# Kernel optimization log

Measured on AMD Instinct MI355X. Metric: run time of the kernel, lower is better.

Reference implementation:

```python
import jax, jax.numpy as jnp
import numpy as np

N = 100000   # nodes
E = 1600000  # edges
D = 256      # emb_dim
H = 512      # 2*emb_dim hidden in GIN MLP
L = 5        # num_layer
NUM_NODE_TYPES = 300
EDGE_FEAT = 7


def setup_inputs() -> dict:
    key = jax.random.key(0)
    ks = jax.random.split(key, 16)
    s = 0.05
    return {
        "x": jax.random.randint(ks[0], (N, 1), 0, NUM_NODE_TYPES, dtype=jnp.int32),
        "edge_index": jax.random.randint(ks[1], (2, E), 0, N, dtype=jnp.int32),
        "edge_attr": jax.random.normal(ks[2], (E, EDGE_FEAT), dtype=jnp.float32),
        "batch": jnp.zeros((N,), dtype=jnp.int32),
        "node_emb": jax.random.normal(ks[3], (NUM_NODE_TYPES, D), dtype=jnp.float32) * s,
        "We": jax.random.normal(ks[4], (L, EDGE_FEAT, D), dtype=jnp.float32) * s,
        "be": jnp.zeros((L, D), dtype=jnp.float32),
        "W1": jax.random.normal(ks[5], (L, D, H), dtype=jnp.float32) * s,
        "b1": jnp.zeros((L, H), dtype=jnp.float32),
        "g1": jnp.ones((L, H), dtype=jnp.float32),
        "bt1": jnp.zeros((L, H), dtype=jnp.float32),
        "W2": jax.random.normal(ks[6], (L, H, D), dtype=jnp.float32) * s,
        "b2": jnp.zeros((L, D), dtype=jnp.float32),
        "eps": jnp.zeros((L,), dtype=jnp.float32),
        "g_bn": jnp.ones((L, D), dtype=jnp.float32),
        "b_bn": jnp.zeros((L, D), dtype=jnp.float32),
    }


def _batchnorm(z, g, b):
    # training-mode BN over the node dim, biased variance, eps=1e-5 (torch default)
    mu = jnp.mean(z, axis=0)
    var = jnp.mean((z - mu) ** 2, axis=0)
    return (z - mu) * jax.lax.rsqrt(var + 1e-5) * g + b


def reference(x, edge_index, edge_attr, batch, node_emb, We, be, W1, b1, g1, bt1,
              W2, b2, eps, g_bn, b_bn):
    src, dst = edge_index[0], edge_index[1]
    h = node_emb[x[:, 0]]                      # [N, D]
    n = h.shape[0]
    for l in range(L):
        edge_emb = edge_attr @ We[l] + be[l]   # [E, D]
        msg = jax.nn.relu(h[src] + edge_emb)   # gather + elementwise message
        agg = jax.ops.segment_sum(msg, dst, num_segments=n)  # scatter-add
        z = (1.0 + eps[l]) * h + agg
        z = jax.nn.relu(_batchnorm(z @ W1[l] + b1[l], g1[l], bt1[l])) @ W2[l] + b2[l]
        z = _batchnorm(z, g_bn[l], b_bn[l])
        h = jax.nn.relu(z) if l != L - 1 else z  # relu on all but last; dropout p=0
    return h  # JK='last'
```

## Files before the change

kernel.cpp:

```cpp
#include <hip/hip_runtime.h>
#include <hip/hip_bf16.h>

#define N_NODES 100000
#define N_EDGES 1600000
#define DIM 256
#define HID 512
#define NLAYERS 5
#define BKP 40
#define MTILES 782

typedef unsigned short u16;
typedef unsigned int u32;
typedef short s16x8 __attribute__((ext_vector_type(8)));
typedef float f32x4 __attribute__((ext_vector_type(4)));

__device__ __forceinline__ float b2f_(u16 u) {
  union { unsigned i; float f; } v;
  v.i = ((unsigned)u) << 16;
  return v.f;
}
__device__ __forceinline__ u16 f2b_(float f) {
  __hip_bfloat16 h = __float2bfloat16(f);
  return *reinterpret_cast<u16*>(&h);
}
__device__ __forceinline__ int pk2_(u16 lo, u16 hi) {
  return (int)(((u32)hi << 16) | (u32)lo);
}
__device__ __forceinline__ void split_pack_(f32x4 a, f32x4 b, int4& hi, int4& lo) {
  float v[8];
  u16 h[8], l[8];
#pragma unroll
  for (int q = 0; q < 4; ++q) { v[q] = a[q]; v[4 + q] = b[q]; }
#pragma unroll
  for (int q = 0; q < 8; ++q) {
    h[q] = f2b_(v[q]);
    l[q] = f2b_(v[q] - b2f_(h[q]));
  }
  hi = make_int4(pk2_(h[0], h[1]), pk2_(h[2], h[3]), pk2_(h[4], h[5]), pk2_(h[6], h[7]));
  lo = make_int4(pk2_(l[0], l[1]), pk2_(l[2], l[3]), pk2_(l[4], l[5]), pk2_(l[6], l[7]));
}
__device__ __forceinline__ int4 bn_pack_(int4 raw, const float* __restrict__ scl,
                                         const float* __restrict__ sft) {
  const u16* rp = (const u16*)&raw;
  u16 o[8];
#pragma unroll
  for (int q = 0; q < 8; ++q) {
    float v = fmaf(b2f_(rp[q]), scl[q], sft[q]);
    o[q] = f2b_(fmaxf(v, 0.f));
  }
  return make_int4(pk2_(o[0], o[1]), pk2_(o[2], o[3]), pk2_(o[4], o[5]), pk2_(o[6], o[7]));
}

__global__ void k_fill(float* out, int n, float val) {
  int i = blockIdx.x * 256 + threadIdx.x;
  if (i < n) out[i] = val;
}

__global__ void k_zero(float* p, int n) {
  int i = blockIdx.x * 256 + threadIdx.x;
  if (i < n) p[i] = 0.f;
}

__global__ void k_zeroi(int* p, int n) {
  int i = blockIdx.x * 256 + threadIdx.x;
  if (i < n) p[i] = 0;
}

__global__ void k_gather(const int* x0, const int* x3, const float* emb, float* h) {
  int idx = blockIdx.x * 256 + threadIdx.x;
  int n = idx >> 8, d = idx & 255;
  int t = x0[n] + x3[n];
  h[idx] = emb[(size_t)t * DIM + d];
}

__global__ void k_hist(const int* __restrict__ dst, int* __restrict__ deg) {
  int e = blockIdx.x * 256 + threadIdx.x;
  if (e < N_EDGES) atomicAdd(&deg[dst[e]], 1);
}

__global__ void k_scan1(const int* __restrict__ deg, int* __restrict__ offs,
                        int* __restrict__ bsum) {
  __shared__ int sm[256];
  int tid = threadIdx.x;
  int i = blockIdx.x * 256 + tid;
  int v = (i < N_NODES) ? deg[i] : 0;
  sm[tid] = v;
  __syncthreads();
  for (int d = 1; d < 256; d <<= 1) {
    int t = (tid >= d) ? sm[tid - d] : 0;
    __syncthreads();
    sm[tid] += t;
    __syncthreads();
  }
  if (i < N_NODES) offs[i] = sm[tid] - v;
  if (tid == 0) bsum[blockIdx.x] = sm[255];
}

__global__ void k_scan2(int* __restrict__ bsum, int nb) {
  __shared__ int sm[512];
  int tid = threadIdx.x;
  int v = (tid < nb) ? bsum[tid] : 0;
  sm[tid] = v;
  __syncthreads();
  for (int d = 1; d < 512; d <<= 1) {
    int t = (tid >= d) ? sm[tid - d] : 0;
    __syncthreads();
    sm[tid] += t;
    __syncthreads();
  }
  if (tid < nb) bsum[tid] = sm[tid] - v;
}

__global__ void k_scan3(int* __restrict__ offs, const int* __restrict__ bsum,
                        int* __restrict__ cur) {
  int i = blockIdx.x * 256 + threadIdx.x;
  if (i < N_NODES) {
    offs[i] += bsum[blockIdx.x];
    cur[i] = 0;
  }
  if (i == 0) offs[N_NODES] = N_EDGES;
}

__global__ void k_fillcsr(const int* __restrict__ dst, const int* __restrict__ srcarr,
                          const float* __restrict__ ea, const int* __restrict__ offs,
                          int* __restrict__ cur, int* __restrict__ elist,
                          float* __restrict__ eaperm) {
  int e = blockIdx.x * 256 + threadIdx.x;
  if (e < N_EDGES) {
    int d = dst[e];
    int p = offs[d] + atomicAdd(&cur[d], 1);
    elist[p] = srcarr[e];
    const float* s = ea + (size_t)e * 7;
    float* o = eaperm + (size_t)p * 7;
#pragma unroll
    for (int k = 0; k < 7; ++k) o[k] = s[k];
  }
}

template <int BNIN>
__global__ __launch_bounds__(256) void k_agg(
    const float* __restrict__ hin, const float* __restrict__ eap,
    const int* __restrict__ csr, const int* __restrict__ offs,
    const float* __restrict__ We, const float* __restrict__ be,
    const float* __restrict__ eps_l, const float* __restrict__ scl2,
    const float* __restrict__ sft2, float* __restrict__ z) {
  const int lane = threadIdx.x & 63;
  const int n = blockIdx.x * 4 + (threadIdx.x >> 6);
  const int c0 = lane * 4;
  float w[7][4];
#pragma unroll
  for (int k = 0; k < 7; ++k) {
    f32x4 t = *(const f32x4*)&We[k * DIM + c0];
    w[k][0] = t[0]; w[k][1] = t[1]; w[k][2] = t[2]; w[k][3] = t[3];
  }
  const f32x4 bev = *(const f32x4*)&be[c0];
  f32x4 sv, fv;
  if (BNIN) { sv = *(const f32x4*)&scl2[c0]; fv = *(const f32x4*)&sft2[c0]; }
  const f32x4 hn = *(const f32x4*)&hin[(size_t)n * DIM + c0];
  const float e1p = 1.0f + eps_l[0];
  float acc[4];
#pragma unroll
  for (int q = 0; q < 4; ++q) {
    float hv = hn[q];
    if (BNIN) hv = fmaxf(fmaf(hv, sv[q], fv[q]), 0.f);
    acc[q] = e1p * hv;
  }

  auto msg = [&](const f32x4& hs, const float* a) {
#pragma unroll
    for (int q = 0; q < 4; ++q) {
      float hv = hs[q];
      if (BNIN) hv = fmaxf(fmaf(hv, sv[q], fv[q]), 0.f);
      float t = bev[q];
#pragma unroll
      for (int k = 0; k < 7; ++k) t = fmaf(a[k], w[k][q], t);
      acc[q] += fmaxf(hv + t, 0.f);
    }
  };

  const int eb = offs[n], ee = offs[n + 1];
  for (int base = eb; base < ee; base += 64) {
    const int m = min(64, ee - base);
    const int cs = csr[base + min(lane, m - 1)];
    int e = 0;
    for (; e + 4 <= m; e += 4) {
      const int s0 = __shfl(cs, e);
      const int s1 = __shfl(cs, e + 1);
      const int s2 = __shfl(cs, e + 2);
      const int s3 = __shfl(cs, e + 3);
      const f32x4 h0 = *(const f32x4*)&hin[(size_t)s0 * DIM + c0];
      const f32x4 h1 = *(const f32x4*)&hin[(size_t)s1 * DIM + c0];
      const f32x4 h2 = *(const f32x4*)&hin[(size_t)s2 * DIM + c0];
      const f32x4 h3 = *(const f32x4*)&hin[(size_t)s3 * DIM + c0];
      const float* p0 = eap + (size_t)(base + e) * 7;
      float a0[7], a1[7], a2[7], a3[7];
#pragma unroll
      for (int k = 0; k < 7; ++k) {
        a0[k] = p0[k]; a1[k] = p0[7 + k]; a2[k] = p0[14 + k]; a3[k] = p0[21 + k];
      }
      msg(h0, a0);
      msg(h1, a1);
      msg(h2, a2);
      msg(h3, a3);
    }
    for (; e < m; ++e) {
      const int s0 = __shfl(cs, e);
      const f32x4 h0 = *(const f32x4*)&hin[(size_t)s0 * DIM + c0];
      const float* p0 = eap + (size_t)(base + e) * 7;
      float a0[7];
#pragma unroll
      for (int k = 0; k < 7; ++k) a0[k] = p0[k];
      msg(h0, a0);
    }
  }
  f32x4 o;
#pragma unroll
  for (int q = 0; q < 4; ++q) o[q] = acc[q];
  *(f32x4*)&z[(size_t)n * DIM + c0] = o;
}

template <int K, int NC>
__global__ void k_wconv(const float* __restrict__ W, u16* __restrict__ Wth,
                        u16* __restrict__ Wtl) {
  int idx = blockIdx.x * 256 + threadIdx.x;
  int n = idx / K, k = idx - n * K;
  float w = W[(size_t)k * NC + n];
  u16 hh = f2b_(w);
  Wth[idx] = hh;
  Wtl[idx] = f2b_(w - b2f_(hh));
}

__global__ void k_bnprep(const float* __restrict__ sum, const float* __restrict__ sq,
                         const float* __restrict__ g, const float* __restrict__ bt,
                         float* __restrict__ scl, float* __restrict__ sft, int n) {
  int j = blockIdx.x * 256 + threadIdx.x;
  if (j < n) {
    const float invN = 1.0f / 100000.0f;
    float mu = sum[j] * invN;
    float var = fmaf(-mu, mu, sq[j] * invN);
    float s = g[j] * rsqrtf(var + 1e-5f);
    scl[j] = s;
    sft[j] = fmaf(-mu, s, bt[j]);
  }
}

template <int K, int NC, int NA, int OBF, int BN1A>
__global__ __launch_bounds__(256) void k_mgemm(
    const void* __restrict__ Av, const u16* __restrict__ Bth,
    const u16* __restrict__ Btl, const float* __restrict__ bias,
    void* __restrict__ Ov, float* __restrict__ colsum, float* __restrict__ colsq,
    const float* __restrict__ ascl, const float* __restrict__ asft) {
  __shared__ u16 As[NA * 128 * BKP];
  __shared__ u16 Bs[2 * 128 * BKP];
  const int tid = threadIdx.x;
  const int m0 = blockIdx.x * 128;
  const int n0 = blockIdx.y * 128;
  const int lane = tid & 63;
  const int wv = tid >> 6;
  const int wr = (wv >> 1) * 64;
  const int wc = (wv & 1) * 64;
  const int lr = lane & 15;
  const int kc = (lane >> 4) * 8;
  const int sr = tid >> 1;
  const int sc = (tid & 1) * 16;
  const int ga = min(m0 + sr, N_NODES - 1);
  const int gb = n0 + sr;

  const f32x4 z4 = {0.f, 0.f, 0.f, 0.f};
  f32x4 acc[4][4];
#pragma unroll
  for (int i = 0; i < 4; ++i)
#pragma unroll
    for (int j = 0; j < 4; ++j) acc[i][j] = z4;

  for (int k0 = 0; k0 < K; k0 += 32) {
    int4 a0, a1, al0, al1;
    if (NA == 2) {
      const float* src = (const float*)Av + (size_t)ga * K + k0 + sc;
      f32x4 v0 = *(const f32x4*)(src);
      f32x4 v1 = *(const f32x4*)(src + 4);
      f32x4 v2 = *(const f32x4*)(src + 8);
      f32x4 v3 = *(const f32x4*)(src + 12);
      split_pack_(v0, v1, a0, al0);
      split_pack_(v2, v3, a1, al1);
    } else {
      const u16* src = (const u16*)Av + (size_t)ga * K + k0 + sc;
      a0 = *(const int4*)(src);
      a1 = *(const int4*)(src + 8);
      if (BN1A) {
        a0 = bn_pack_(a0, ascl + k0 + sc, asft + k0 + sc);
        a1 = bn_pack_(a1, ascl + k0 + sc + 8, asft + k0 + sc + 8);
      }
    }
    const u16* bhp = Bth + (size_t)gb * K + k0 + sc;
    const u16* blp = Btl + (size_t)gb * K + k0 + sc;
    int4 b0 = *(const int4*)(bhp);
    int4 b1 = *(const int4*)(bhp + 8);
    int4 b2 = *(const int4*)(blp);
    int4 b3 = *(const int4*)(blp + 8);

    __syncthreads();
    *(int4*)&As[sr * BKP + sc] = a0;
    *(int4*)&As[sr * BKP + sc + 8] = a1;
    if (NA == 2) {
      *(int4*)&As[128 * BKP + sr * BKP + sc] = al0;
      *(int4*)&As[128 * BKP + sr * BKP + sc + 8] = al1;
    }
    *(int4*)&Bs[sr * BKP + sc] = b0;
    *(int4*)&Bs[sr * BKP + sc + 8] = b1;
    *(int4*)&Bs[128 * BKP + sr * BKP + sc] = b2;
    *(int4*)&Bs[128 * BKP + sr * BKP + sc + 8] = b3;
    __syncthreads();

    s16x8 aF[NA][4], bF[2][4];
#pragma unroll
    for (int i = 0; i < 4; ++i) {
      aF[0][i] = *reinterpret_cast<const s16x8*>(&As[(wr + i * 16 + lr) * BKP + kc]);
      if (NA == 2)
        aF[1][i] =
            *reinterpret_cast<const s16x8*>(&As[128 * BKP + (wr + i * 16 + lr) * BKP + kc]);
      bF[0][i] = *reinterpret_cast<const s16x8*>(&Bs[(wc + i * 16 + lr) * BKP + kc]);
      bF[1][i] = *reinterpret_cast<const s16x8*>(&Bs[128 * BKP + (wc + i * 16 + lr) * BKP + kc]);
    }
#pragma unroll
    for (int i = 0; i < 4; ++i)
#pragma unroll
      for (int j = 0; j < 4; ++j) {
        acc[i][j] =
            __builtin_amdgcn_mfma_f32_16x16x32_bf16(aF[0][i], bF[0][j], acc[i][j], 0, 0, 0);
        acc[i][j] =
            __builtin_amdgcn_mfma_f32_16x16x32_bf16(aF[0][i], bF[1][j], acc[i][j], 0, 0, 0);
        if (NA == 2)
          acc[i][j] =
              __builtin_amdgcn_mfma_f32_16x16x32_bf16(aF[1][i], bF[0][j], acc[i][j], 0, 0, 0);
      }
  }

  float bj[4];
#pragma unroll
  for (int j = 0; j < 4; ++j) bj[j] = bias[n0 + wc + j * 16 + lr];
  float ls[4] = {0.f, 0.f, 0.f, 0.f}, lq[4] = {0.f, 0.f, 0.f, 0.f};
#pragma unroll
  for (int i = 0; i < 4; ++i) {
    const int row0 = m0 + wr + i * 16 + (lane >> 4) * 4;
#pragma unroll
    for (int r = 0; r < 4; ++r) {
      const int grow = row0 + r;
      if (grow < N_NODES) {
        const size_t o = (size_t)grow * NC + n0 + wc + lr;
#pragma unroll
        for (int j = 0; j < 4; ++j) {
          float v = acc[i][j][r] + bj[j];
          ls[j] += v;
          lq[j] = fmaf(v, v, lq[j]);
          if (OBF) ((u16*)Ov)[o + j * 16] = f2b_(v);
          else ((float*)Ov)[o + j * 16] = v;
        }
      }
    }
  }
#pragma unroll
  for (int j = 0; j < 4; ++j) {
    float s = ls[j], q = lq[j];
    s += __shfl_xor(s, 16); q += __shfl_xor(q, 16);
    s += __shfl_xor(s, 32); q += __shfl_xor(q, 32);
    if ((lane >> 4) == 0) {
      unsafeAtomicAdd(&colsum[n0 + wc + j * 16 + lr], s);
      unsafeAtomicAdd(&colsq[n0 + wc + j * 16 + lr], q);
    }
  }
}

__global__ void k_bn(const void* Y, int y_bf, const float* sum, const float* sq,
                     const float* g, const float* b, int NC_mask,
                     void* O, int o_bf, int do_relu) {
  int idx = blockIdx.x * 256 + threadIdx.x;
  int j = idx & NC_mask;
  const float invN = 1.0f / 100000.0f;
  float mu = sum[j] * invN;
  float var = fmaf(-mu, mu, sq[j] * invN);
  float v = y_bf ? b2f_(((const u16*)Y)[idx]) : ((const float*)Y)[idx];
  v = fmaf((v - mu) * rsqrtf(var + 1e-5f), g[j], b[j]);
  if (do_relu) v = fmaxf(v, 0.f);
  if (o_bf) ((u16*)O)[idx] = f2b_(v);
  else ((float*)O)[idx] = v;
}

extern "C" void kernel_launch(void* const* d_in, const int* in_sizes, int n_in,
                              void* d_out, int out_size, void* d_ws, size_t ws_size,
                              hipStream_t stream) {
  float* out = (float*)d_out;

  const int expected[16] = {100000, 3200000, 11200000, 100000, 76800, 8960, 1280,
                            655360, 2560, 2560, 2560, 655360, 1280, 5, 1280, 1280};
  float sentinel = 0.f;
  if (n_in != 16) sentinel = 60.f;
  else
    for (int i = 0; i < 16; ++i)
      if (in_sizes[i] != expected[i]) { sentinel = 100.f + (float)i; break; }
  if (sentinel == 0.f && out_size != N_NODES * DIM) sentinel = 90.f;

  const size_t ND = (size_t)N_NODES * DIM;
  const size_t NH = (size_t)N_NODES * HID;
  const size_t base = 4096 * sizeof(float);
  const size_t need_base = base + 2 * ND * sizeof(float) + NH * sizeof(u16);
  if (sentinel == 0.f && ws_size < need_base) sentinel = 77.f;
  if (sentinel != 0.f) {
    k_fill<<<(out_size + 255) / 256, 256, 0, stream>>>(out, out_size, sentinel);
    return;
  }

  float* stats = (float*)d_ws;
  float* sum1 = stats;
  float* sq1 = sum1 + HID;
  float* sum2 = sq1 + HID;
  float* sq2 = sum2 + DIM;
  float* scl1 = stats + 1536;
  float* sft1 = scl1 + HID;
  float* scl2 = sft1 + HID;
  float* sft2 = scl2 + DIM;
  float* bufA = stats + 4096;
  float* bufB = bufA + ND;
  u16* Y1 = (u16*)(bufB + ND);

  const size_t csr_ints =
      (size_t)N_NODES + (size_t)(N_NODES + 1) + 512 + 1 + (size_t)N_EDGES;
  const size_t csr_bytes = csr_ints * sizeof(int) + (size_t)N_EDGES * 7 * sizeof(float);
  const int csr_tail = ws_size >= need_base + csr_bytes;
  int* degc = csr_tail ? (int*)((char*)d_ws + need_base) : (int*)Y1;
  int* offs = degc + N_NODES;
  int* bsum = offs + N_NODES + 1;
  int* elist = bsum + 512 + 1;
  float* eaperm = (float*)(elist + N_EDGES);
  const int NB_N = (N_NODES + 255) / 256;
  const int NB_E = N_EDGES / 256;

  const int* x0 = (const int*)d_in[0];
  const int* ei = (const int*)d_in[1];
  const float* ea = (const float*)d_in[2];
  const int* x3 = (const int*)d_in[3];
  const float* emb = (const float*)d_in[4];
  const float* We = (const float*)d_in[5];
  const float* be = (const float*)d_in[6];
  const float* W1 = (const float*)d_in[7];
  const float* b1 = (const float*)d_in[8];
  const float* g1 = (const float*)d_in[9];
  const float* bt1 = (const float*)d_in[10];
  const float* W2 = (const float*)d_in[11];
  const float* b2 = (const float*)d_in[12];
  const float* eps = (const float*)d_in[13];
  const float* g_bn = (const float*)d_in[14];
  const float* b_bn = (const float*)d_in[15];

  const int* srcs = ei;
  const int* dsts = ei + N_EDGES;

  const int gridND = (int)(ND / 256);

  auto build_csr = [&]() {
    k_zeroi<<<NB_N, 256, 0, stream>>>(degc, N_NODES);
    k_hist<<<NB_E, 256, 0, stream>>>(dsts, degc);
    k_scan1<<<NB_N, 256, 0, stream>>>(degc, offs, bsum);
    k_scan2<<<1, 512, 0, stream>>>(bsum, NB_N);
    k_scan3<<<NB_N, 256, 0, stream>>>(offs, bsum, degc);
    k_fillcsr<<<NB_E, 256, 0, stream>>>(dsts, srcs, ea, offs, degc, elist, eaperm);
  };

  k_gather<<<gridND, 256, 0, stream>>>(x0, x3, emb, bufA);
  if (csr_tail) build_csr();

  float* bufs[2] = {bufA, bufB};
  int p = 0;
  for (int l = 0; l < NLAYERS; ++l) {
    float* IN = bufs[p];
    float* ZB = bufs[1 - p];
    u16* Wth = (u16*)IN;
    u16* Wtl = Wth + (size_t)DIM * HID;

    if (!csr_tail) build_csr();
    k_zero<<<6, 256, 0, stream>>>(stats, 1536);

    if (l == 0)
      k_agg<0><<<N_NODES / 4, 256, 0, stream>>>(IN, eaperm, elist, offs,
                                                We + (size_t)l * 7 * DIM,
                                                be + (size_t)l * DIM, eps + l,
                                                nullptr, nullptr, ZB);
    else
      k_agg<1><<<N_NODES / 4, 256, 0, stream>>>(IN, eaperm, elist, offs,
                                                We + (size_t)l * 7 * DIM,
                                                be + (size_t)l * DIM, eps + l,
                                                scl2, sft2, ZB);

    k_wconv<DIM, HID><<<(DIM * HID) / 256, 256, 0, stream>>>(
        W1 + (size_t)l * DIM * HID, Wth, Wtl);
    k_mgemm<DIM, HID, 2, 1, 0><<<dim3(MTILES, HID / 128), 256, 0, stream>>>(
        ZB, Wth, Wtl, b1 + (size_t)l * HID, Y1, sum1, sq1, nullptr, nullptr);
    k_bnprep<<<2, 256, 0, stream>>>(sum1, sq1, g1 + (size_t)l * HID,
                                    bt1 + (size_t)l * HID, scl1, sft1, HID);

    k_wconv<HID, DIM><<<(DIM * HID) / 256, 256, 0, stream>>>(
        W2 + (size_t)l * HID * DIM, Wth, Wtl);
    k_mgemm<HID, DIM, 1, 0, 1><<<dim3(MTILES, DIM / 128), 256, 0, stream>>>(
        Y1, Wth, Wtl, b2 + (size_t)l * DIM, ZB, sum2, sq2, scl1, sft1);

    if (l != NLAYERS - 1)
      k_bnprep<<<1, 256, 0, stream>>>(sum2, sq2, g_bn + (size_t)l * DIM,
                                      b_bn + (size_t)l * DIM, scl2, sft2, DIM);
    else
      k_bn<<<gridND, 256, 0, stream>>>(ZB, 0, sum2, sq2, g_bn + (size_t)l * DIM,
                                       b_bn + (size_t)l * DIM, DIM - 1, out, 0, 0);
    p ^= 1;
  }
}
```

Measured before the change: 3.248 ms.

## Split aggregates to bf16 hi/lo in k_agg and stream GEMM tiles into swizzled LDS

```diff
diff --git a/kernel.cpp b/kernel.cpp
--- a/kernel.cpp
+++ b/kernel.cpp
@@ -6,7 +6,6 @@
 #define DIM 256
 #define HID 512
 #define NLAYERS 5
-#define BKP 40
 #define MTILES 782
 
 typedef unsigned short u16;
@@ -26,19 +25,6 @@
 __device__ __forceinline__ int pk2_(u16 lo, u16 hi) {
   return (int)(((u32)hi << 16) | (u32)lo);
 }
-__device__ __forceinline__ void split_pack_(f32x4 a, f32x4 b, int4& hi, int4& lo) {
-  float v[8];
-  u16 h[8], l[8];
-#pragma unroll
-  for (int q = 0; q < 4; ++q) { v[q] = a[q]; v[4 + q] = b[q]; }
-#pragma unroll
-  for (int q = 0; q < 8; ++q) {
-    h[q] = f2b_(v[q]);
-    l[q] = f2b_(v[q] - b2f_(h[q]));
-  }
-  hi = make_int4(pk2_(h[0], h[1]), pk2_(h[2], h[3]), pk2_(h[4], h[5]), pk2_(h[6], h[7]));
-  lo = make_int4(pk2_(l[0], l[1]), pk2_(l[2], l[3]), pk2_(l[4], l[5]), pk2_(l[6], l[7]));
-}
 __device__ __forceinline__ int4 bn_pack_(int4 raw, const float* __restrict__ scl,
                                          const float* __restrict__ sft) {
   const u16* rp = (const u16*)&raw;
@@ -49,6 +35,16 @@
     o[q] = f2b_(fmaxf(v, 0.f));
   }
   return make_int4(pk2_(o[0], o[1]), pk2_(o[2], o[3]), pk2_(o[4], o[5]), pk2_(o[6], o[7]));
+}
+
+__device__ __forceinline__ void gl16_(const u16* g, u16* l) {
+  __builtin_amdgcn_global_load_lds(
+      (const __attribute__((address_space(1))) void*)g,
+      (__attribute__((address_space(3))) void*)l, 16, 0, 0);
+}
+
+__device__ __forceinline__ int lds_off(int row, int g) {
+  return row * 32 + (((g ^ (row >> 1)) & 3) << 3);
 }
 
 __global__ void k_fill(float* out, int n, float val) {
@@ -143,7 +139,7 @@
     const int* __restrict__ csr, const int* __restrict__ offs,
     const float* __restrict__ We, const float* __restrict__ be,
     const float* __restrict__ eps_l, const float* __restrict__ scl2,
-    const float* __restrict__ sft2, float* __restrict__ z) {
+    const float* __restrict__ sft2, u16* __restrict__ zh, u16* __restrict__ zl) {
   const int lane = threadIdx.x & 63;
   const int n = blockIdx.x * 4 + (threadIdx.x >> 6);
   const int c0 = lane * 4;
@@ -213,10 +209,16 @@
       msg(h0, a0);
     }
   }
-  f32x4 o;
-#pragma unroll
-  for (int q = 0; q < 4; ++q) o[q] = acc[q];
-  *(f32x4*)&z[(size_t)n * DIM + c0] = o;
+  ushort4 zh4, zl4;
+#pragma unroll
+  for (int q = 0; q < 4; ++q) {
+    u16 hh = f2b_(acc[q]);
+    float lo = acc[q] - b2f_(hh);
+    ((u16*)&zh4)[q] = hh;
+    ((u16*)&zl4)[q] = f2b_(lo);
+  }
+  *(ushort4*)&zh[(size_t)n * DIM + c0] = zh4;
+  *(ushort4*)&zl[(size_t)n * DIM + c0] = zl4;
 }
 
 template <int K, int NC>
@@ -246,12 +248,13 @@
 
 template <int K, int NC, int NA, int OBF, int BN1A>
 __global__ __launch_bounds__(256) void k_mgemm(
-    const void* __restrict__ Av, const u16* __restrict__ Bth,
-    const u16* __restrict__ Btl, const float* __restrict__ bias,
-    void* __restrict__ Ov, float* __restrict__ colsum, float* __restrict__ colsq,
+    const u16* __restrict__ Ah, const u16* __restrict__ Al,
+    const u16* __restrict__ Bth, const u16* __restrict__ Btl,
+    const float* __restrict__ bias, void* __restrict__ Ov,
+    float* __restrict__ colsum, float* __restrict__ colsq,
     const float* __restrict__ ascl, const float* __restrict__ asft) {
-  __shared__ u16 As[NA * 128 * BKP];
-  __shared__ u16 Bs[2 * 128 * BKP];
+  __shared__ u16 As[NA * 128 * 32];
+  __shared__ u16 Bs[2 * 128 * 32];
   const int tid = threadIdx.x;
   const int m0 = blockIdx.x * 128;
   const int n0 = blockIdx.y * 128;
@@ -260,11 +263,12 @@
   const int wr = (wv >> 1) * 64;
   const int wc = (wv & 1) * 64;
   const int lr = lane & 15;
-  const int kc = (lane >> 4) * 8;
+  const int g = lane >> 4;
   const int sr = tid >> 1;
   const int sc = (tid & 1) * 16;
   const int ga = min(m0 + sr, N_NODES - 1);
-  const int gb = n0 + sr;
+  const int grow16 = lane >> 2;
+  const int glc = (lane & 3) ^ ((lane >> 3) & 3);
 
   const f32x4 z4 = {0.f, 0.f, 0.f, 0.f};
   f32x4 acc[4][4];
@@ -274,53 +278,54 @@
     for (int j = 0; j < 4; ++j) acc[i][j] = z4;
 
   for (int k0 = 0; k0 < K; k0 += 32) {
-    int4 a0, a1, al0, al1;
-    if (NA == 2) {
-      const float* src = (const float*)Av + (size_t)ga * K + k0 + sc;
-      f32x4 v0 = *(const f32x4*)(src);
-      f32x4 v1 = *(const f32x4*)(src + 4);
-      f32x4 v2 = *(const f32x4*)(src + 8);
-      f32x4 v3 = *(const f32x4*)(src + 12);
-      split_pack_(v0, v1, a0, al0);
-      split_pack_(v2, v3, a1, al1);
-    } else {
-      const u16* src = (const u16*)Av + (size_t)ga * K + k0 + sc;
-      a0 = *(const int4*)(src);
-      a1 = *(const int4*)(src + 8);
+    int4 a0, a1;
+    if (NA == 1) {
+      const u16* srcp = Ah + (size_t)ga * K + k0 + sc;
+      a0 = *(const int4*)(srcp);
+      a1 = *(const int4*)(srcp + 8);
       if (BN1A) {
         a0 = bn_pack_(a0, ascl + k0 + sc, asft + k0 + sc);
         a1 = bn_pack_(a1, ascl + k0 + sc + 8, asft + k0 + sc + 8);
       }
     }
-    const u16* bhp = Bth + (size_t)gb * K + k0 + sc;
-    const u16* blp = Btl + (size_t)gb * K + k0 + sc;
-    int4 b0 = *(const int4*)(bhp);
-    int4 b1 = *(const int4*)(bhp + 8);
-    int4 b2 = *(const int4*)(blp);
-    int4 b3 = *(const int4*)(blp + 8);
-
     __syncthreads();
-    *(int4*)&As[sr * BKP + sc] = a0;
-    *(int4*)&As[sr * BKP + sc + 8] = a1;
     if (NA == 2) {
-      *(int4*)&As[128 * BKP + sr * BKP + sc] = al0;
-      *(int4*)&As[128 * BKP + sr * BKP + sc + 8] = al1;
-    }
-    *(int4*)&Bs[sr * BKP + sc] = b0;
-    *(int4*)&Bs[sr * BKP + sc + 8] = b1;
-    *(int4*)&Bs[128 * BKP + sr * BKP + sc] = b2;
-    *(int4*)&Bs[128 * BKP + sr * BKP + sc + 8] = b3;
+      const u16* gbase;
+      u16* lbase;
+      int rbase, rclamp;
+      if (wv == 0)      { gbase = Ah;  lbase = As;        rbase = m0; rclamp = N_NODES - 1; }
+      else if (wv == 1) { gbase = Al;  lbase = As + 4096; rbase = m0; rclamp = N_NODES - 1; }
+      else if (wv == 2) { gbase = Bth; lbase = Bs;        rbase = n0; rclamp = 0x7fffffff; }
+      else              { gbase = Btl; lbase = Bs + 4096; rbase = n0; rclamp = 0x7fffffff; }
+#pragma unroll
+      for (int c = 0; c < 8; ++c) {
+        int gr = min(rbase + c * 16 + grow16, rclamp);
+        gl16_(gbase + (size_t)gr * K + k0 + glc * 8, lbase + c * 512);
+      }
+    } else {
+      const int x = (sr >> 1) & 3;
+      const int lc0 = (tid & 1) * 2;
+      *(int4*)&As[sr * 32 + ((lc0 ^ x) << 3)] = a0;
+      *(int4*)&As[sr * 32 + (((lc0 + 1) ^ x) << 3)] = a1;
+      const u16* gbase = (wv >> 1) ? Btl : Bth;
+      u16* lbase = (wv >> 1) ? Bs + 4096 : Bs;
+#pragma unroll
+      for (int cc = 0; cc < 4; ++cc) {
+        int c = (wv & 1) * 4 + cc;
+        int gr = n0 + c * 16 + grow16;
+        gl16_(gbase + (size_t)gr * K + k0 + glc * 8, lbase + c * 512);
+      }
+    }
     __syncthreads();
 
     s16x8 aF[NA][4], bF[2][4];
 #pragma unroll
     for (int i = 0; i < 4; ++i) {
-      aF[0][i] = *reinterpret_cast<const s16x8*>(&As[(wr + i * 16 + lr) * BKP + kc]);
+      aF[0][i] = *reinterpret_cast<const s16x8*>(&As[lds_off(wr + i * 16 + lr, g)]);
       if (NA == 2)
-        aF[1][i] =
-            *reinterpret_cast<const s16x8*>(&As[128 * BKP + (wr + i * 16 + lr) * BKP + kc]);
-      bF[0][i] = *reinterpret_cast<const s16x8*>(&Bs[(wc + i * 16 + lr) * BKP + kc]);
-      bF[1][i] = *reinterpret_cast<const s16x8*>(&Bs[128 * BKP + (wc + i * 16 + lr) * BKP + kc]);
+        aF[1][i] = *reinterpret_cast<const s16x8*>(&As[4096 + lds_off(wr + i * 16 + lr, g)]);
+      bF[0][i] = *reinterpret_cast<const s16x8*>(&Bs[lds_off(wc + i * 16 + lr, g)]);
+      bF[1][i] = *reinterpret_cast<const s16x8*>(&Bs[4096 + lds_off(wc + i * 16 + lr, g)]);
     }
 #pragma unroll
     for (int i = 0; i < 4; ++i)
@@ -474,6 +479,8 @@
   for (int l = 0; l < NLAYERS; ++l) {
     float* IN = bufs[p];
     float* ZB = bufs[1 - p];
+    u16* zh = (u16*)ZB;
+    u16* zl = zh + ND;
     u16* Wth = (u16*)IN;
     u16* Wtl = Wth + (size_t)DIM * HID;
 
@@ -484,24 +491,24 @@
       k_agg<0><<<N_NODES / 4, 256, 0, stream>>>(IN, eaperm, elist, offs,
                                                 We + (size_t)l * 7 * DIM,
                                                 be + (size_t)l * DIM, eps + l,
-                                                nullptr, nullptr, ZB);
+                                                nullptr, nullptr, zh, zl);
     else
       k_agg<1><<<N_NODES / 4, 256, 0, stream>>>(IN, eaperm, elist, offs,
                                                 We + (size_t)l * 7 * DIM,
                                                 be + (size_t)l * DIM, eps + l,
-                                                scl2, sft2, ZB);
+                                                scl2, sft2, zh, zl);
 
     k_wconv<DIM, HID><<<(DIM * HID) / 256, 256, 0, stream>>>(
         W1 + (size_t)l * DIM * HID, Wth, Wtl);
     k_mgemm<DIM, HID, 2, 1, 0><<<dim3(MTILES, HID / 128), 256, 0, stream>>>(
-        ZB, Wth, Wtl, b1 + (size_t)l * HID, Y1, sum1, sq1, nullptr, nullptr);
+        zh, zl, Wth, Wtl, b1 + (size_t)l * HID, Y1, sum1, sq1, nullptr, nullptr);
     k_bnprep<<<2, 256, 0, stream>>>(sum1, sq1, g1 + (size_t)l * HID,
                                     bt1 + (size_t)l * HID, scl1, sft1, HID);
 
     k_wconv<HID, DIM><<<(DIM * HID) / 256, 256, 0, stream>>>(
         W2 + (size_t)l * HID * DIM, Wth, Wtl);
     k_mgemm<HID, DIM, 1, 0, 1><<<dim3(MTILES, DIM / 128), 256, 0, stream>>>(
-        Y1, Wth, Wtl, b2 + (size_t)l * DIM, ZB, sum2, sq2, scl1, sft1);
+        Y1, nullptr, Wth, Wtl, b2 + (size_t)l * DIM, ZB, sum2, sq2, scl1, sft1);
 
     if (l != NLAYERS - 1)
       k_bnprep<<<1, 256, 0, stream>>>(sum2, sq2, g_bn + (size_t)l * DIM,
```

New measurement: 3.274 ms. About the same (+0.8%).
